# Performance work log

Measured on AMD Instinct MI355X. Metric: run time of the kernel, lower is better.

Reference implementation:

```python
import jax, jax.numpy as jnp
import numpy as np

N_NODES = 100000
D = 64        # graph_embed_size == utterance_embed_size
B = 64        # batch size == number of groups per layer
K = 500000    # selected candidate nodes per layer
M = 200000    # mention nodes
ATT_H = 20    # attention_hidden_dim
CTX = 4 * D   # context_embed_size = 2*graph + 2*utter


def setup_inputs() -> dict:
    key = jax.random.key(0)
    ks = jax.random.split(key, 16)
    graph_embed = jax.random.normal(ks[0], (N_NODES, D), jnp.float32)
    utterance_embed = jax.random.normal(ks[1], (B, D), jnp.float32)
    mention_index = jax.random.randint(ks[2], (M,), 0, N_NODES)
    mention_batch_index = jnp.sort(jax.random.randint(ks[3], (M,), 0, B))
    sel_indices = jax.random.randint(ks[4], (2, K), 0, N_NODES + 1)
    sel_batch_indices = jnp.sort(jax.random.randint(ks[5], (2, K), 0, B), axis=-1)
    sel_group_indices = jnp.sort(jax.random.randint(ks[6], (2, K), 0, B), axis=-1)
    grp_batch_indices = jnp.tile(jnp.arange(B), (2, 1))  # group i belongs to batch i
    last_indices = jax.random.randint(ks[7], (2, B), 0, N_NODES + 1)
    intent_indices = jax.random.randint(ks[8], (2, B), 0, 3)
    score_masks = jnp.ones((2, K), jnp.float32)
    # learned parameters (torch nn.Linear default init: U(-1/sqrt(fan_in), 1/sqrt(fan_in)))
    s_w = 1.0 / np.sqrt(D)
    s_v = 1.0 / np.sqrt(ATT_H)
    s_c = 1.0 / np.sqrt(CTX)
    att_W = jax.random.uniform(ks[9], (ATT_H, D), jnp.float32, -s_w, s_w)
    att_V = jax.random.uniform(ks[10], (1, ATT_H), jnp.float32, -s_v, s_v)
    W1_w = jax.random.uniform(ks[11], (1, CTX), jnp.float32, -s_c, s_c)
    W1_b = jax.random.uniform(ks[12], (1,), jnp.float32, -s_c, s_c)
    W2_w = jax.random.uniform(ks[13], (1, CTX), jnp.float32, -s_c, s_c)
    W2_b = jax.random.uniform(ks[14], (1,), jnp.float32, -s_c, s_c)
    intent_emb = jax.random.normal(ks[15], (3, D), jnp.float32)
    return dict(graph_embed=graph_embed, utterance_embed=utterance_embed,
                mention_index=mention_index, mention_batch_index=mention_batch_index,
                sel_indices=sel_indices, sel_batch_indices=sel_batch_indices,
                sel_group_indices=sel_group_indices, grp_batch_indices=grp_batch_indices,
                last_indices=last_indices, intent_indices=intent_indices,
                score_masks=score_masks, att_W=att_W, att_V=att_V,
                W1_w=W1_w, W1_b=W1_b, W2_w=W2_w, W2_b=W2_b, intent_emb=intent_emb)


def _segment_attention(embed, batch_index, att_W, att_V):
    # Self_Attention with batch_index: segment softmax + weighted segment sum.
    beta = jnp.squeeze(jnp.tanh(embed @ att_W.T) @ att_V.T, -1)      # [M]
    exp_beta = jnp.exp(beta)                                          # faithful: raw exp
    seg_sum = jax.ops.segment_sum(exp_beta, batch_index, num_segments=B)  # [B]
    alpha = exp_beta / seg_sum[batch_index]                           # [M]
    return jax.ops.segment_sum(alpha[:, None] * embed, batch_index, num_segments=B)  # [B,D]


def _layer(W_w, W_b, utter, portrait, graph_e, sel, sel_b, sel_g, grp_b,
           last, intent, mask, intent_emb, last_weight):
    context = jnp.concatenate([utter, portrait], axis=-1)             # [B,2D]
    feats = graph_e[sel]                                              # [K,D]
    # grp_context = [tiled context | start-point embed | intent embed] -> [G,4D]
    grp_ctx = jnp.concatenate([context[grp_b], graph_e[last], intent_emb[intent]], axis=-1)
    weights = jax.nn.sigmoid(grp_ctx @ W_w.T + W_b)                   # [G,1]
    tu = utter[sel_b]                                                 # [K,D]
    tp = portrait[sel_b]                                              # [K,D]
    w = weights[sel_g]                                                # [K,1]
    scores = jnp.sum((tu * w + tp * (1.0 - w)) * feats, axis=-1)      # [K]
    if last_weight is None:
        return scores, weights
    lw = last_weight[sel_b]                                           # [K,1]
    last_scores = jnp.sum((tu * lw + tp * (1.0 - lw)) * feats, axis=-1)
    return last_scores + mask * scores, None


def reference(graph_embed, utterance_embed, mention_index, mention_batch_index,
              sel_indices, sel_batch_indices, sel_group_indices, grp_batch_indices,
              last_indices, intent_indices, score_masks,
              att_W, att_V, W1_w, W1_b, W2_w, W2_b, intent_emb):
    # user portrait via segment-softmax attention over mentioned nodes
    mention_embed = graph_embed[mention_index]                        # [M,D]
    portrait = _segment_attention(mention_embed, mention_batch_index, att_W, att_V)  # [B,D]
    # extended graph embedding with abstract (zero) row appended
    graph_e = jnp.concatenate([graph_embed, jnp.zeros((1, D), graph_embed.dtype)], axis=0)
    s0, w0 = _layer(W1_w, W1_b, utterance_embed, portrait, graph_e,
                    sel_indices[0], sel_batch_indices[0], sel_group_indices[0],
                    grp_batch_indices[0], last_indices[0], intent_indices[0],
                    score_masks[0], intent_emb, None)
    s1, _ = _layer(W2_w, W2_b, utterance_embed, portrait, graph_e,
                   sel_indices[1], sel_batch_indices[1], sel_group_indices[1],
                   grp_batch_indices[1], last_indices[1], intent_indices[1],
                   score_masks[1], intent_emb, w0)
    return jnp.stack([s0, s1], axis=0)                                # [2,K]
```

## Files before the change

kernel.cpp:

```cpp
#include <hip/hip_runtime.h>
#include <math.h>

#define N_NODES 100000
#define D_EMB   64
#define KSEL    500000
#define NMENT   200000
#define ATT_H   20
#define NPAD    100008

#define WS_EB    0
#define WS_NUM   100000
#define WS_DEN   104096
#define WS_PORT  104160
#define WS_W     108256
#define WS_KCODE 108384
#define WS_MCODE 1108384
#define WS_BF_FLOAT_OFF 1308416
#define WS_BF_BYTE ((size_t)WS_BF_FLOAT_OFF * 4)
#define WS_T     4508416
#define WS_TOTAL_BYTES ((size_t)(WS_T + 64 * NPAD) * 4)

#define NPB 391
#define MCB 196
#define KCB 977

typedef __attribute__((ext_vector_type(8))) short bf16x8;
typedef __attribute__((ext_vector_type(4))) float f32x4;

__device__ __forceinline__ unsigned pack2bf(float a, float b) {
    unsigned ua = __float_as_uint(a), ub = __float_as_uint(b);
    ua = (ua + 0x7FFFu + ((ua >> 16) & 1u)) >> 16;
    ub = (ub + 0x7FFFu + ((ub >> 16) & 1u)) >> 16;
    return ua | (ub << 16);
}
__device__ __forceinline__ float uasf(unsigned u) { return __uint_as_float(u); }

template<bool PACK>
__global__ __launch_bounds__(256) void kP(const float* __restrict__ ge,
                                          const float* __restrict__ attW,
                                          const float* __restrict__ attV,
                                          const int* __restrict__ mi,
                                          const int* __restrict__ mbi,
                                          const int* __restrict__ sel,
                                          const int* __restrict__ selb,
                                          const int* __restrict__ selg,
                                          float* __restrict__ ws) {
    int bid = blockIdx.x;
    if (PACK && bid >= NPB) {
        int t = threadIdx.x;
        if (bid < NPB + MCB) {
            int base = (bid - NPB) * 1024 + t * 4;
            int* mc = (int*)ws + WS_MCODE;
            if (base + 3 < NMENT) {
                int4 a = *(const int4*)(mi + base);
                int4 b = *(const int4*)(mbi + base);
                int4 o;
                o.x = a.x | (b.x << 17); o.y = a.y | (b.y << 17);
                o.z = a.z | (b.z << 17); o.w = a.w | (b.w << 17);
                *(int4*)(mc + base) = o;
            } else {
                for (int i = base; i < NMENT; ++i) mc[i] = mi[i] | (mbi[i] << 17);
            }
        } else {
            int base = (bid - NPB - MCB) * 1024 + t * 4;
            int* kc = (int*)ws + WS_KCODE;
            if (base + 3 < 2 * KSEL) {
                int4 a = *(const int4*)(sel + base);
                int4 b = *(const int4*)(selb + base);
                int4 g = *(const int4*)(selg + base);
                int4 o;
                o.x = a.x | (b.x << 17) | (g.x << 23);
                o.y = a.y | (b.y << 17) | (g.y << 23);
                o.z = a.z | (b.z << 17) | (g.z << 23);
                o.w = a.w | (b.w << 17) | (g.w << 23);
                *(int4*)(kc + base) = o;
            } else {
                for (int i = base; i < 2 * KSEL; ++i)
                    kc[i] = sel[i] | (selb[i] << 17) | (selg[i] << 23);
            }
        }
        return;
    }

    int tid = bid * 256 + threadIdx.x;
    if (tid < 64 * 64 + 64) ws[WS_NUM + tid] = 0.f;
    if (tid >= N_NODES) return;

    const float4* g4 = (const float4*)(ge + (size_t)tid * D_EMB);
    float4 x[16];
#pragma unroll
    for (int i = 0; i < 16; ++i) x[i] = g4[i];

    if constexpr (PACK) {
        uint4* dst = (uint4*)((char*)ws + WS_BF_BYTE + (size_t)tid * 128);
#pragma unroll
        for (int j = 0; j < 8; ++j) {
            uint4 o;
            o.x = pack2bf(x[2*j].x,   x[2*j].y);
            o.y = pack2bf(x[2*j].z,   x[2*j].w);
            o.z = pack2bf(x[2*j+1].x, x[2*j+1].y);
            o.w = pack2bf(x[2*j+1].z, x[2*j+1].w);
            dst[j] = o;
        }
    }

    float beta = 0.f;
#pragma unroll
    for (int j = 0; j < ATT_H; ++j) {
        float h = 0.f;
#pragma unroll
        for (int i = 0; i < 16; ++i) {
            float4 w = ((const float4*)(attW + j * D_EMB))[i];
            h += w.x * x[i].x + w.y * x[i].y + w.z * x[i].z + w.w * x[i].w;
        }
        beta += attV[j] * tanhf(h);
    }
    ws[WS_EB + tid] = expf(beta);
}

__global__ __launch_bounds__(256, 8) void kA2n(float* __restrict__ ws) {
    __shared__ float lacc[64 * 64];
    __shared__ float lden[64];
    for (int i = threadIdx.x; i < 64 * 64; i += 256) lacc[i] = 0.f;
    if (threadIdx.x < 64) lden[threadIdx.x] = 0.f;
    __syncthreads();

    const int* mc = (const int*)ws + WS_MCODE;
    const unsigned short* bft = (const unsigned short*)((const char*)ws + WS_BF_BYTE);

    int lane = threadIdx.x & 63;
    int grp  = lane >> 4, lp = lane & 15;
    int wave = blockIdx.x * 4 + (threadIdx.x >> 6);
    int s = wave * 25;

    int cd[7]; float ebv[7]; uint2 rr[7];
#pragma unroll
    for (int i = 0; i < 7; ++i) {
        bool v = (4 * i + grp) < 25;
        cd[i] = v ? mc[s + 4 * i + grp] : 0;
    }
#pragma unroll
    for (int i = 0; i < 7; ++i) {
        bool v = (4 * i + grp) < 25;
        int nd = cd[i] & 0x1FFFF;
        ebv[i] = v ? ws[WS_EB + nd] : 0.f;
        rr[i]  = *(const uint2*)(bft + (size_t)nd * 64 + lp * 4);
    }

    int curb = (cd[0] >> 17) & 63;
    float4 acc = make_float4(0.f, 0.f, 0.f, 0.f);
    float dacc = 0.f;
#pragma unroll
    for (int i = 0; i < 7; ++i) {
        int b = (cd[i] >> 17) & 63;
        bool v = (4 * i + grp) < 25;
        if (v && b != curb) {
            atomicAdd(&lacc[curb * 64 + lp * 4 + 0], acc.x);
            atomicAdd(&lacc[curb * 64 + lp * 4 + 1], acc.y);
            atomicAdd(&lacc[curb * 64 + lp * 4 + 2], acc.z);
            atomicAdd(&lacc[curb * 64 + lp * 4 + 3], acc.w);
            if (lp == 0) atomicAdd(&lden[curb], dacc);
            acc = make_float4(0.f, 0.f, 0.f, 0.f); dacc = 0.f; curb = b;
        }
        float e = ebv[i];
        acc.x = fmaf(e, uasf(rr[i].x << 16),         acc.x);
        acc.y = fmaf(e, uasf(rr[i].x & 0xFFFF0000u), acc.y);
        acc.z = fmaf(e, uasf(rr[i].y << 16),         acc.z);
        acc.w = fmaf(e, uasf(rr[i].y & 0xFFFF0000u), acc.w);
        dacc += e;
    }
    atomicAdd(&lacc[curb * 64 + lp * 4 + 0], acc.x);
    atomicAdd(&lacc[curb * 64 + lp * 4 + 1], acc.y);
    atomicAdd(&lacc[curb * 64 + lp * 4 + 2], acc.z);
    atomicAdd(&lacc[curb * 64 + lp * 4 + 3], acc.w);
    if (lp == 0) atomicAdd(&lden[curb], dacc);
    __syncthreads();

    int sB = blockIdx.x * 100;
    int b0 = (mc[sB] >> 17) & 63;
    int b1 = (mc[sB + 99] >> 17) & 63;
    int nb = b1 - b0 + 1;
    for (int idx = threadIdx.x; idx < nb * 64; idx += 256) {
        int bb = b0 + (idx >> 6), d = idx & 63;
        float v = lacc[bb * 64 + d];
        if (v != 0.f) atomicAdd(&ws[WS_NUM + bb * 64 + d], v);
    }
    if (threadIdx.x < nb) {
        float v = lden[b0 + threadIdx.x];
        if (v != 0.f) atomicAdd(&ws[WS_DEN + b0 + threadIdx.x], v);
    }
}

__global__ __launch_bounds__(64) void kBW(const float* __restrict__ ge,
                                          const float* __restrict__ utter,
                                          const int* __restrict__ grpb,
                                          const int* __restrict__ lastI,
                                          const int* __restrict__ intentI,
                                          const float* __restrict__ W1w,
                                          const float* __restrict__ W1b,
                                          const float* __restrict__ W2w,
                                          const float* __restrict__ W2b,
                                          const float* __restrict__ intentEmb,
                                          float* __restrict__ ws) {
    int bi = blockIdx.x;
    int l  = bi >> 6;
    int g  = bi & 63;
    int d  = threadIdx.x;

    if (l == 0) {
        ws[WS_PORT + g * 64 + d] = ws[WS_NUM + g * 64 + d] / ws[WS_DEN + g];
    }
    int gb = grpb[bi];
    float pd = ws[WS_NUM + gb * 64 + d] / ws[WS_DEN + gb];

    int last = lastI[bi];
    float gl = (last < N_NODES) ? ge[(size_t)last * D_EMB + d] : 0.f;
    int it = intentI[bi];
    float ie = intentEmb[it * D_EMB + d];

    const float* Ww = (l == 0) ? W1w : W2w;
    float bias      = (l == 0) ? W1b[0] : W2b[0];

    float val = utter[gb * D_EMB + d] * Ww[d]
              + pd * Ww[64 + d]
              + gl * Ww[128 + d]
              + ie * Ww[192 + d];
#pragma unroll
    for (int off = 32; off; off >>= 1) val += __shfl_xor(val, off);
    if (d == 0) ws[WS_W + bi] = 1.f / (1.f + expf(-(val + bias)));
}

__global__ __launch_bounds__(256) void kG(const float* __restrict__ ge,
                                          const float* __restrict__ utter,
                                          float* __restrict__ ws) {
    __shared__ unsigned sQ[128 * 36];
    __shared__ unsigned sT[4][16 * 65];

    int tid = threadIdx.x;
    for (int i = tid; i < 128 * 32; i += 256) {
        int q = i >> 5, c32 = i & 31;
        int k2 = c32 * 2;
        float a, b;
        if (q < 64) { a = utter[q * 64 + k2];               b = utter[q * 64 + k2 + 1]; }
        else        { a = ws[WS_PORT + (q - 64) * 64 + k2]; b = ws[WS_PORT + (q - 64) * 64 + k2 + 1]; }
        sQ[q * 36 + c32] = pack2bf(a, b);
    }
    __syncthreads();

    int l = tid & 63, w = tid >> 6;
    int r16 = l & 15, kb = l >> 4;

    bf16x8 Bf[8][2];
#pragma unroll
    for (int c = 0; c < 8; ++c)
#pragma unroll
        for (int s = 0; s < 2; ++s) {
            int q = c * 16 + r16;
            uint4 u = *(const uint4*)&sQ[q * 36 + s * 16 + kb * 4];
            Bf[c][s] = __builtin_bit_cast(bf16x8, u);
        }

    unsigned* Tu = (unsigned*)(ws + WS_T);

#pragma unroll 1
    for (int t = 0; t < 4; ++t) {
        int nb0 = blockIdx.x * 256 + t * 64 + w * 16;
        int node = nb0 + r16;
        bf16x8 Af[2];
#pragma unroll
        for (int s = 0; s < 2; ++s) {
            uint4 u = make_uint4(0u, 0u, 0u, 0u);
            if (node < N_NODES) {
                const float* p = ge + (size_t)node * 64 + s * 32 + kb * 8;
                float4 p0 = *(const float4*)p;
                float4 p1 = *(const float4*)(p + 4);
                u = make_uint4(pack2bf(p0.x, p0.y), pack2bf(p0.z, p0.w),
                               pack2bf(p1.x, p1.y), pack2bf(p1.z, p1.w));
            }
            Af[s] = __builtin_bit_cast(bf16x8, u);
        }

        f32x4 acc[8];
#pragma unroll
        for (int c = 0; c < 8; ++c) acc[c] = (f32x4){0.f, 0.f, 0.f, 0.f};
#pragma unroll
        for (int s = 0; s < 2; ++s)
#pragma unroll
            for (int c = 0; c < 8; ++c)
                acc[c] = __builtin_amdgcn_mfma_f32_16x16x32_bf16(Af[s], Bf[c][s], acc[c], 0, 0, 0);

#pragma unroll
        for (int c = 0; c < 4; ++c)
#pragma unroll
            for (int r = 0; r < 4; ++r)
                sT[w][(kb * 4 + r) * 65 + (c * 16 + r16)] = pack2bf(acc[c][r], acc[c + 4][r]);
        __syncthreads();

#pragma unroll
        for (int it = 0; it < 16; ++it) {
            int idx = it * 64 + l;
            int b = idx >> 4, nn = idx & 15;
            int node2 = blockIdx.x * 256 + t * 64 + w * 16 + nn;
            if (node2 < NPAD)
                Tu[(size_t)b * NPAD + node2] = sT[w][nn * 65 + b];
        }
        __syncthreads();
    }
}

__global__ __launch_bounds__(256) void kS(const float* __restrict__ masks,
                                          const float* __restrict__ ws,
                                          float* __restrict__ out) {
    __shared__ float sWd[128];
    if (threadIdx.x < 128) sWd[threadIdx.x] = ws[WS_W + threadIdx.x];
    __syncthreads();
    int kk = blockIdx.x * 256 + threadIdx.x;
    if (kk >= 2 * KSEL) return;
    const int* kc = (const int*)ws + WS_KCODE;
    int code = kc[kk];
    int n = code & 0x1FFFF, b = (code >> 17) & 63, g = (code >> 23) & 63;
    const unsigned* Tu = (const unsigned*)(ws + WS_T);
    unsigned t = Tu[(size_t)b * NPAD + n];
    float du = uasf(t << 16), dp = uasf(t & 0xFFFF0000u);
    float cu, cp;
    if (kk < KSEL) {
        float wv = sWd[g]; cu = wv; cp = 1.f - wv;
    } else {
        float mk = masks[kk];
        float lw = sWd[b], w1 = sWd[64 + g];
        cu = fmaf(mk, w1, lw);
        cp = fmaf(mk, 1.f - w1, 1.f - lw);
    }
    out[kk] = cu * du + cp * dp;
}

#define KA2_L 25
__global__ __launch_bounds__(256) void kA2_fb(const float* __restrict__ ge,
                                              const int* __restrict__ mi,
                                              const int* __restrict__ mbi,
                                              float* __restrict__ ws) {
    int lane = threadIdx.x & 63;
    int wave = (blockIdx.x * 256 + threadIdx.x) >> 6;
    int wstart = wave * KA2_L;
    if (wstart >= NMENT) return;
    int wend = min(wstart + KA2_L, NMENT);
    int len  = wend - wstart;

    int idx    = wstart + lane;
    bool valid = idx < wend;
    int lastB  = mbi[wend - 1];
    int nd     = valid ? mi[idx] : 0;
    int bb     = valid ? mbi[idx] : lastB;
    float ebv  = valid ? ws[WS_EB + nd] : 0.f;
    int code   = nd | (bb << 17);

    float acc = 0.f, dacc = 0.f;
    int curb = __shfl(code, 0) >> 17;

    int Lr = (len + 3) & ~3;
    for (int u0 = 0; u0 < Lr; u0 += 4) {
        int c4[4]; float e4[4]; float x4[4];
#pragma unroll
        for (int j = 0; j < 4; ++j) {
            int u = u0 + j;
            c4[j] = __shfl(code, u);
            e4[j] = __shfl(ebv, u);
            x4[j] = ge[(size_t)(c4[j] & 0x1FFFF) * D_EMB + lane];
        }
#pragma unroll
        for (int j = 0; j < 4; ++j) {
            int b = c4[j] >> 17;
            if (b != curb) {
                atomicAdd(&ws[WS_NUM + curb * 64 + lane], acc);
                if (lane == 0) atomicAdd(&ws[WS_DEN + curb], dacc);
                acc = 0.f; dacc = 0.f; curb = b;
            }
            acc  = fmaf(e4[j], x4[j], acc);
            dacc += e4[j];
        }
    }
    atomicAdd(&ws[WS_NUM + curb * 64 + lane], acc);
    if (lane == 0) atomicAdd(&ws[WS_DEN + curb], dacc);
}

__global__ __launch_bounds__(512, 8) void kC_fb(const float* __restrict__ ge,
                                                const float* __restrict__ utter,
                                                const int* __restrict__ sel,
                                                const int* __restrict__ selb,
                                                const int* __restrict__ selg,
                                                const float* __restrict__ masks,
                                                const float* __restrict__ ws,
                                                float* __restrict__ out) {
    __shared__ float4 sU[64 * 17];
    __shared__ float4 sP[64 * 17];
    __shared__ float  sW[128];
    for (int i = threadIdx.x; i < 64 * 16; i += 512) {
        int r = i >> 4, c = i & 15;
        sU[r * 17 + c] = ((const float4*)utter)[i];
        sP[r * 17 + c] = ((const float4*)(ws + WS_PORT))[i];
    }
    if (threadIdx.x < 128) sW[threadIdx.x] = ws[WS_W + threadIdx.x];
    __syncthreads();

    int lane = threadIdx.x & 63;
    int wave = blockIdx.x * 8 + (threadIdx.x >> 6);
    int W = gridDim.x * 8;
    int grp = lane >> 4, lp = lane & 15;
    const float4* g4 = (const float4*)ge;
    const int NGRP = 2 * KSEL / 4;

    for (int gi = wave; gi < NGRP; gi += W) {
        int kk = gi * 4 + grp;
        int node = sel[kk], b = selb[kk], g = selg[kk];
        float cu, cp;
        if (kk < KSEL) { float w = sW[g]; cu = w; cp = 1.f - w; }
        else {
            float mask = masks[kk]; float lw = sW[b]; float w1 = sW[64 + g];
            cu = fmaf(mask, w1, lw); cp = fmaf(mask, 1.f - w1, 1.f - lw);
        }
        float4 f = make_float4(0.f, 0.f, 0.f, 0.f);
        if (node < N_NODES) f = g4[(size_t)node * 16 + lp];
        float4 tu = sU[b * 17 + lp];
        float4 tp = sP[b * 17 + lp];
        float val = (cu * tu.x + cp * tp.x) * f.x
                  + (cu * tu.y + cp * tp.y) * f.y
                  + (cu * tu.z + cp * tp.z) * f.z
                  + (cu * tu.w + cp * tp.w) * f.w;
        val += __shfl_xor(val, 1);
        val += __shfl_xor(val, 2);
        val += __shfl_xor(val, 4);
        val += __shfl_xor(val, 8);
        if (lp == 0) out[kk] = val;
    }
}

extern "C" void kernel_launch(void* const* d_in, const int* in_sizes, int n_in,
                              void* d_out, int out_size, void* d_ws, size_t ws_size,
                              hipStream_t stream) {
    const float* ge        = (const float*)d_in[0];
    const float* utter     = (const float*)d_in[1];
    const int*   mi        = (const int*)d_in[2];
    const int*   mbi       = (const int*)d_in[3];
    const int*   sel       = (const int*)d_in[4];
    const int*   selb      = (const int*)d_in[5];
    const int*   selg      = (const int*)d_in[6];
    const int*   grpb      = (const int*)d_in[7];
    const int*   lastI     = (const int*)d_in[8];
    const int*   intentI   = (const int*)d_in[9];
    const float* masks     = (const float*)d_in[10];
    const float* attW      = (const float*)d_in[11];
    const float* attV      = (const float*)d_in[12];
    const float* W1w       = (const float*)d_in[13];
    const float* W1b       = (const float*)d_in[14];
    const float* W2w       = (const float*)d_in[15];
    const float* W2b       = (const float*)d_in[16];
    const float* intentEmb = (const float*)d_in[17];
    float* ws  = (float*)d_ws;
    float* out = (float*)d_out;

    bool full = ws_size >= WS_TOTAL_BYTES;

    if (full) {
        kP<true><<<dim3(NPB + MCB + KCB), dim3(256), 0, stream>>>(
            ge, attW, attV, mi, mbi, sel, selb, selg, ws);
        kA2n<<<dim3(2000), dim3(256), 0, stream>>>(ws);
        kBW<<<dim3(128), dim3(64), 0, stream>>>(ge, utter, grpb, lastI, intentI,
                                                W1w, W1b, W2w, W2b, intentEmb, ws);
        kG<<<dim3((NPAD + 255) / 256 + 1), dim3(256), 0, stream>>>(ge, utter, ws);
        kS<<<dim3((2 * KSEL + 255) / 256), dim3(256), 0, stream>>>(masks, ws, out);
    } else {
        kP<false><<<dim3(NPB), dim3(256), 0, stream>>>(
            ge, attW, attV, mi, mbi, sel, selb, selg, ws);
        kA2_fb<<<dim3(2000), dim3(256), 0, stream>>>(ge, mi, mbi, ws);
        kBW<<<dim3(128), dim3(64), 0, stream>>>(ge, utter, grpb, lastI, intentI,
                                                W1w, W1b, W2w, W2b, intentEmb, ws);
        kC_fb<<<dim3(1024), dim3(512), 0, stream>>>(ge, utter, sel, selb, selg,
                                                    masks, ws, out);
    }
}
```

Before: 92.41 us.

## Fuse gate computation into projection kernel and store results directly without LDS transpose

The separate gate-weight kernel (kBW) is folded into the last block of the bf16 MFMA projection kernel kG, removing one launch from the fast path. The portrait is computed inline as numerator over denominator instead of being read back from a stored buffer. The LDS transpose and its two barriers are replaced by direct 16-byte stores from the MFMA accumulators. NPAD is raised to 100352 so these vector stores stay aligned and in bounds, which enlarges the workspace and could push the code onto the slower fallback if the provided workspace is too small.

```diff
diff --git a/kernel.cpp b/kernel.cpp
--- a/kernel.cpp
+++ b/kernel.cpp
@@ -6,7 +6,7 @@
 #define KSEL    500000
 #define NMENT   200000
 #define ATT_H   20
-#define NPAD    100008
+#define NPAD    100352
 
 #define WS_EB    0
 #define WS_NUM   100000
@@ -23,6 +23,7 @@
 #define NPB 391
 #define MCB 196
 #define KCB 977
+#define NBLK_G 784
 
 typedef __attribute__((ext_vector_type(8))) short bf16x8;
 typedef __attribute__((ext_vector_type(4))) float f32x4;
@@ -191,7 +192,7 @@
     }
 }
 
-__global__ __launch_bounds__(64) void kBW(const float* __restrict__ ge,
+__global__ __launch_bounds__(256) void kG(const float* __restrict__ ge,
                                           const float* __restrict__ utter,
                                           const int* __restrict__ grpb,
                                           const int* __restrict__ lastI,
@@ -202,47 +203,43 @@
                                           const float* __restrict__ W2b,
                                           const float* __restrict__ intentEmb,
                                           float* __restrict__ ws) {
-    int bi = blockIdx.x;
-    int l  = bi >> 6;
-    int g  = bi & 63;
-    int d  = threadIdx.x;
-
-    if (l == 0) {
-        ws[WS_PORT + g * 64 + d] = ws[WS_NUM + g * 64 + d] / ws[WS_DEN + g];
-    }
-    int gb = grpb[bi];
-    float pd = ws[WS_NUM + gb * 64 + d] / ws[WS_DEN + gb];
-
-    int last = lastI[bi];
-    float gl = (last < N_NODES) ? ge[(size_t)last * D_EMB + d] : 0.f;
-    int it = intentI[bi];
-    float ie = intentEmb[it * D_EMB + d];
-
-    const float* Ww = (l == 0) ? W1w : W2w;
-    float bias      = (l == 0) ? W1b[0] : W2b[0];
-
-    float val = utter[gb * D_EMB + d] * Ww[d]
-              + pd * Ww[64 + d]
-              + gl * Ww[128 + d]
-              + ie * Ww[192 + d];
-#pragma unroll
-    for (int off = 32; off; off >>= 1) val += __shfl_xor(val, off);
-    if (d == 0) ws[WS_W + bi] = 1.f / (1.f + expf(-(val + bias)));
-}
-
-__global__ __launch_bounds__(256) void kG(const float* __restrict__ ge,
-                                          const float* __restrict__ utter,
-                                          float* __restrict__ ws) {
+    int bid = blockIdx.x;
+    if (bid == NBLK_G - 1) {
+        int w = threadIdx.x >> 6, d = threadIdx.x & 63;
+#pragma unroll 2
+        for (int bi = w; bi < 128; bi += 4) {
+            int l = bi >> 6, g = bi & 63;
+            int gb = grpb[bi];
+            float pd = ws[WS_NUM + gb * 64 + d] / ws[WS_DEN + gb];
+            int last = lastI[bi];
+            float gl = (last < N_NODES) ? ge[(size_t)last * 64 + d] : 0.f;
+            float ie = intentEmb[intentI[bi] * 64 + d];
+            const float* Ww = l ? W2w : W1w;
+            float bias      = l ? W2b[0] : W1b[0];
+            float val = utter[gb * 64 + d] * Ww[d]
+                      + pd * Ww[64 + d]
+                      + gl * Ww[128 + d]
+                      + ie * Ww[192 + d];
+#pragma unroll
+            for (int off = 32; off; off >>= 1) val += __shfl_xor(val, off);
+            if (d == 0) ws[WS_W + bi] = 1.f / (1.f + expf(-(val + bias)));
+        }
+        return;
+    }
+
     __shared__ unsigned sQ[128 * 36];
-    __shared__ unsigned sT[4][16 * 65];
-
     int tid = threadIdx.x;
     for (int i = tid; i < 128 * 32; i += 256) {
         int q = i >> 5, c32 = i & 31;
         int k2 = c32 * 2;
         float a, b;
-        if (q < 64) { a = utter[q * 64 + k2];               b = utter[q * 64 + k2 + 1]; }
-        else        { a = ws[WS_PORT + (q - 64) * 64 + k2]; b = ws[WS_PORT + (q - 64) * 64 + k2 + 1]; }
+        if (q < 64) {
+            a = utter[q * 64 + k2]; b = utter[q * 64 + k2 + 1];
+        } else {
+            float dn = ws[WS_DEN + q - 64];
+            a = ws[WS_NUM + (q - 64) * 64 + k2] / dn;
+            b = ws[WS_NUM + (q - 64) * 64 + k2 + 1] / dn;
+        }
         sQ[q * 36 + c32] = pack2bf(a, b);
     }
     __syncthreads();
@@ -263,8 +260,8 @@
     unsigned* Tu = (unsigned*)(ws + WS_T);
 
 #pragma unroll 1
-    for (int t = 0; t < 4; ++t) {
-        int nb0 = blockIdx.x * 256 + t * 64 + w * 16;
+    for (int t = 0; t < 2; ++t) {
+        int nb0 = bid * 128 + w * 32 + t * 16;
         int node = nb0 + r16;
         bf16x8 Af[2];
 #pragma unroll
@@ -290,21 +287,15 @@
                 acc[c] = __builtin_amdgcn_mfma_f32_16x16x32_bf16(Af[s], Bf[c][s], acc[c], 0, 0, 0);
 
 #pragma unroll
-        for (int c = 0; c < 4; ++c)
-#pragma unroll
-            for (int r = 0; r < 4; ++r)
-                sT[w][(kb * 4 + r) * 65 + (c * 16 + r16)] = pack2bf(acc[c][r], acc[c + 4][r]);
-        __syncthreads();
-
-#pragma unroll
-        for (int it = 0; it < 16; ++it) {
-            int idx = it * 64 + l;
-            int b = idx >> 4, nn = idx & 15;
-            int node2 = blockIdx.x * 256 + t * 64 + w * 16 + nn;
-            if (node2 < NPAD)
-                Tu[(size_t)b * NPAD + node2] = sT[w][nn * 65 + b];
-        }
-        __syncthreads();
+        for (int c = 0; c < 4; ++c) {
+            uint4 o;
+            o.x = pack2bf(acc[c][0], acc[c + 4][0]);
+            o.y = pack2bf(acc[c][1], acc[c + 4][1]);
+            o.z = pack2bf(acc[c][2], acc[c + 4][2]);
+            o.w = pack2bf(acc[c][3], acc[c + 4][3]);
+            int b = c * 16 + r16;
+            *(uint4*)(Tu + (size_t)b * NPAD + nb0 + kb * 4) = o;
+        }
     }
 }
 
@@ -332,6 +323,45 @@
         cp = fmaf(mk, 1.f - w1, 1.f - lw);
     }
     out[kk] = cu * du + cp * dp;
+}
+
+__global__ __launch_bounds__(64) void kBW(const float* __restrict__ ge,
+                                          const float* __restrict__ utter,
+                                          const int* __restrict__ grpb,
+                                          const int* __restrict__ lastI,
+                                          const int* __restrict__ intentI,
+                                          const float* __restrict__ W1w,
+                                          const float* __restrict__ W1b,
+                                          const float* __restrict__ W2w,
+                                          const float* __restrict__ W2b,
+                                          const float* __restrict__ intentEmb,
+                                          float* __restrict__ ws) {
+    int bi = blockIdx.x;
+    int l  = bi >> 6;
+    int g  = bi & 63;
+    int d  = threadIdx.x;
+
+    if (l == 0) {
+        ws[WS_PORT + g * 64 + d] = ws[WS_NUM + g * 64 + d] / ws[WS_DEN + g];
+    }
+    int gb = grpb[bi];
+    float pd = ws[WS_NUM + gb * 64 + d] / ws[WS_DEN + gb];
+
+    int last = lastI[bi];
+    float gl = (last < N_NODES) ? ge[(size_t)last * D_EMB + d] : 0.f;
+    int it = intentI[bi];
+    float ie = intentEmb[it * D_EMB + d];
+
+    const float* Ww = (l == 0) ? W1w : W2w;
+    float bias      = (l == 0) ? W1b[0] : W2b[0];
+
+    float val = utter[gb * D_EMB + d] * Ww[d]
+              + pd * Ww[64 + d]
+              + gl * Ww[128 + d]
+              + ie * Ww[192 + d];
+#pragma unroll
+    for (int off = 32; off; off >>= 1) val += __shfl_xor(val, off);
+    if (d == 0) ws[WS_W + bi] = 1.f / (1.f + expf(-(val + bias)));
 }
 
 #define KA2_L 25
@@ -464,9 +494,8 @@
         kP<true><<<dim3(NPB + MCB + KCB), dim3(256), 0, stream>>>(
             ge, attW, attV, mi, mbi, sel, selb, selg, ws);
         kA2n<<<dim3(2000), dim3(256), 0, stream>>>(ws);
-        kBW<<<dim3(128), dim3(64), 0, stream>>>(ge, utter, grpb, lastI, intentI,
-                                                W1w, W1b, W2w, W2b, intentEmb, ws);
-        kG<<<dim3((NPAD + 255) / 256 + 1), dim3(256), 0, stream>>>(ge, utter, ws);
+        kG<<<dim3(NBLK_G), dim3(256), 0, stream>>>(ge, utter, grpb, lastI, intentI,
+                                                   W1w, W1b, W2w, W2b, intentEmb, ws);
         kS<<<dim3((2 * KSEL + 255) / 256), dim3(256), 0, stream>>>(masks, ws, out);
     } else {
         kP<false><<<dim3(NPB), dim3(256), 0, stream>>>(
```

Measured after the change: 113.3 us. 22.6% more time.
